# Kernel optimization log

Measured on AMD Instinct MI355X. Metric: run time of the kernel, lower is better.

## Reference

```python
import jax, jax.numpy as jnp
import numpy as np

T, B, F, H, P = 256, 512, 256, 512, 12  # seq len, batch, feature_dim, hidden_dim, p_interval


def setup_inputs() -> dict:
    key = jax.random.key(0)
    ks = jax.random.split(key, 9)
    s = 1.0 / np.sqrt(F + H)  # torch Linear default init scale
    def lin(k):
        kw, kb = jax.random.split(k)
        W = jax.random.uniform(kw, (F + H, H), jnp.float32, -s, s)
        b = jax.random.uniform(kb, (H,), jnp.float32, -s, s)
        return W, b
    Wf, bf = lin(ks[0])
    Wi, bi = lin(ks[1])
    Wo, bo = lin(ks[2])
    Wg, bg = lin(ks[3])
    x = jax.random.normal(ks[4], (T, B, F), jnp.float32)
    return {"x": x, "Wf": Wf, "bf": bf, "Wi": Wi, "bi": bi,
            "Wo": Wo, "bo": bo, "Wg": Wg, "bg": bg}


def _slstm(x, Wf, bf, Wi, bi, Wo, bo, Wg, bg):
    Tn, Bn, _ = x.shape
    h0 = jnp.zeros((P, Bn, H), x.dtype)
    # NOTE: original torch code reassigns c to a 2D [B,H] tensor after step 0,
    # so c[t % P] indexes a batch ROW (shape [H]) that broadcasts. At t=0 the
    # slice is all-zeros either way, so carrying a 2D c is exactly faithful.
    c0 = jnp.zeros((Bn, H), x.dtype)

    def step(carry, inp):
        h, c = carry
        x_t, t = inp
        idx = t % P
        xc = jnp.concatenate([x_t, h[idx]], axis=1)  # [B, F+H]
        f = jax.nn.softmax(xc @ Wf + bf, axis=1)
        i = jax.nn.softmax(xc @ Wi + bi, axis=1)
        o = jax.nn.softmax(xc @ Wo + bo, axis=1)
        g = jnp.tanh(xc @ Wg + bg)
        c_new = jnp.tanh(f * c[idx] + i * g)  # c[idx]: row [H], broadcasts over B
        h = h.at[idx].set(o * c_new)
        return (h, c_new), None

    (h, _), _ = jax.lax.scan(step, (h0, c0), (x, jnp.arange(Tn)))
    return h[(Tn - 1) % P]


def reference(x, Wf, bf, Wi, bi, Wo, bo, Wg, bg):
    return _slstm(x, Wf, bf, Wi, bi, Wo, bo, Wg, bg)
```

## Files before the change

kernel.cpp:

```cpp
#include <hip/hip_runtime.h>

typedef unsigned short u16;
typedef unsigned int   u32;

typedef __attribute__((ext_vector_type(8))) short bf16x8;
typedef __attribute__((ext_vector_type(16))) float f32x16;

__device__ __forceinline__ u16 f2bf(float v) {
    u32 u = __float_as_uint(v);
    u32 r = (u + 0x7fffu + ((u >> 16) & 1u)) >> 16;
    return (u16)r;
}
__device__ __forceinline__ float bf2f(u16 h) { return __uint_as_float(((u32)h) << 16); }

__device__ __forceinline__ float ftanh(float x) {
    float e = __expf(2.0f * x);
    return 1.0f - 2.0f * __builtin_amdgcn_rcpf(e + 1.0f);
}

__device__ __forceinline__ void gl2lds16(const void* g, void* l) {
    __builtin_amdgcn_global_load_lds(
        (const __attribute__((address_space(1))) void*)g,
        (__attribute__((address_space(3))) void*)l, 16, 0, 0);
}

__global__ void init_k(u16* __restrict__ hh, u16* __restrict__ hl, float* __restrict__ cb) {
    int i = blockIdx.x * 256 + threadIdx.x;
    hh[i] = 0; hl[i] = 0;
    if (i < 2 * 512) cb[i] = 0.0f;
}

__global__ void pack_wq(const float* __restrict__ Wf, const float* __restrict__ bf_,
                        const float* __restrict__ Wi, const float* __restrict__ bi_,
                        const float* __restrict__ Wo, const float* __restrict__ bo_,
                        const float* __restrict__ Wg, const float* __restrict__ bg_,
                        u16* __restrict__ wq, float* __restrict__ bias4) {
    int idx = blockIdx.x * 256 + threadIdx.x;
    int n = idx / 768, k = idx - n * 768;
    int gate = n >> 9, col = n & 511;
    const float* W = (gate == 0) ? Wf : (gate == 1) ? Wi : (gate == 2) ? Wo : Wg;
    float v = W[k * 512 + col];
    u16 h = f2bf(v);
    u16 l = f2bf(v - bf2f(h));
    size_t base = (size_t)n * 2304;
    if (k < 256) {
        wq[base + k] = h; wq[base + 512 + k] = h; wq[base + 256 + k] = l;
    } else {
        int d = k - 256;
        wq[base + 768 + d] = h; wq[base + 1792 + d] = h; wq[base + 1280 + d] = l;
    }
    if (k == 0) {
        const float* bb = (gate == 0) ? bf_ : (gate == 1) ? bi_ : (gate == 2) ? bo_ : bg_;
        bias4[n] = bb[col];
    }
}

__global__ void split_x(const float* __restrict__ src, u16* __restrict__ oh, u16* __restrict__ ol) {
    int i = blockIdx.x * 256 + threadIdx.x;
    float4 v = ((const float4*)src)[i];
    u16 hx = f2bf(v.x), hy = f2bf(v.y), hz = f2bf(v.z), hw = f2bf(v.w);
    u16 lx = f2bf(v.x - bf2f(hx)), ly = f2bf(v.y - bf2f(hy));
    u16 lz = f2bf(v.z - bf2f(hz)), lw = f2bf(v.w - bf2f(hw));
    uint2 hv; hv.x = (u32)hx | ((u32)hy << 16); hv.y = (u32)hz | ((u32)hw << 16);
    uint2 lv; lv.x = (u32)lx | ((u32)ly << 16); lv.y = (u32)lz | ((u32)lw << 16);
    ((uint2*)oh)[i] = hv;
    ((uint2*)ol)[i] = lv;
}

#define KT 36
__global__ __launch_bounds__(512, 2) void gemm_q(
    const u16* __restrict__ xh, const u16* __restrict__ xl,
    const u16* __restrict__ hh, const u16* __restrict__ hl,
    const u16* __restrict__ wq, const float* __restrict__ bias4,
    float* __restrict__ lg, int Mvalid, int gx) {
    __shared__ __align__(16) u16 smem[69632];

    const int tid = threadIdx.x;
    const int wid = tid >> 6, lane = tid & 63;
    const int l32 = lane & 31, khalf = lane >> 5;
    const int wm = wid >> 2, wn = wid & 3;

    int bm, bn;
    if (gx == 32) { int xcd = blockIdx.x & 7, r = blockIdx.x >> 3; bm = xcd * 4 + (r & 3); bn = r >> 2; }
    else          { bm = blockIdx.x % gx; bn = blockIdx.x / gx; }

    const int lr8 = lane >> 3;
    const int ksw = ((lane & 7) ^ (lr8 & 7)) * 8;

    int arowc[3]; size_t brow[4];
#pragma unroll
    for (int c = 0; c < 3; ++c) {
        int row = bm * 192 + (wid * 3 + c) * 8 + lr8;
        if (row >= Mvalid) row = Mvalid - 1;
        arowc[c] = row;
    }
#pragma unroll
    for (int c = 0; c < 4; ++c)
        brow[c] = (size_t)(bn * 256 + (wid * 4 + c) * 8 + lr8) * 2304;

#define STAGE_A(kt, dstoff) do {                                              \
        int kt_ = (kt); const u16* base_; int str_, ko_;                      \
        if (kt_ < 12) { base_ = (kt_ >= 8) ? xl : xh; str_ = 256; ko_ = (kt_ & 3) * 64; } \
        else { int sub_ = kt_ - 12; base_ = (sub_ >= 16) ? hl : hh; str_ = 512; ko_ = (sub_ & 7) * 64; } \
        _Pragma("unroll")                                                     \
        for (int c_ = 0; c_ < 3; ++c_)                                        \
            gl2lds16(base_ + (size_t)arowc[c_] * str_ + ko_ + ksw,            \
                     smem + (dstoff) + (wid * 3 + c_) * 512 + lane * 8);      \
    } while (0)

#define STAGE_B(kt, dstoff) do {                                              \
        _Pragma("unroll")                                                     \
        for (int c_ = 0; c_ < 4; ++c_)                                        \
            gl2lds16(wq + brow[c_] + (kt) * 64 + ksw,                         \
                     smem + (dstoff) + (wid * 4 + c_) * 512 + lane * 8);      \
    } while (0)

    u32 offA[3][4], offB[2][4];
#pragma unroll
    for (int i = 0; i < 3; ++i) {
        int row = wm * 96 + i * 32 + l32;
        u32 rsw = (u32)(row & 7) << 3;
#pragma unroll
        for (int ks = 0; ks < 4; ++ks)
            offA[i][ks] = (u32)row * 64 + (((u32)(ks * 16 + khalf * 8)) ^ rsw);
    }
#pragma unroll
    for (int j = 0; j < 2; ++j) {
        int row = wn * 64 + j * 32 + l32;
        u32 rsw = (u32)(row & 7) << 3;
#pragma unroll
        for (int ks = 0; ks < 4; ++ks)
            offB[j][ks] = (u32)row * 64 + (((u32)(ks * 16 + khalf * 8)) ^ rsw);
    }

    f32x16 acc[3][2];
#pragma unroll
    for (int i = 0; i < 3; ++i)
#pragma unroll
        for (int j = 0; j < 2; ++j)
#pragma unroll
            for (int r = 0; r < 16; ++r) acc[i][j][r] = 0.f;

    STAGE_A(0, 0);
    STAGE_B(0, 36864);
    STAGE_A(1, 12288);

    int aoff = 0;
    for (int kt = 0; kt < KT; ++kt) {
        const int boff = 36864 + ((kt & 1) << 14);
        if (kt + 1 < KT) {
            STAGE_B(kt + 1, 36864 + (((kt + 1) & 1) << 14));
            asm volatile("s_waitcnt vmcnt(7)" ::: "memory");
        } else {
            asm volatile("s_waitcnt vmcnt(0)" ::: "memory");
        }
        __builtin_amdgcn_s_barrier();
        __builtin_amdgcn_sched_barrier(0);

        const u16* At = smem + aoff;
        const u16* Bt = smem + boff;

        bf16x8 a0[3][2], b0[2][2];
#pragma unroll
        for (int i = 0; i < 3; ++i)
#pragma unroll
            for (int ks = 0; ks < 2; ++ks) a0[i][ks] = *(const bf16x8*)(At + offA[i][ks]);
#pragma unroll
        for (int j = 0; j < 2; ++j)
#pragma unroll
            for (int ks = 0; ks < 2; ++ks) b0[j][ks] = *(const bf16x8*)(Bt + offB[j][ks]);
        __builtin_amdgcn_s_setprio(1);
#pragma unroll
        for (int ks = 0; ks < 2; ++ks)
#pragma unroll
            for (int i = 0; i < 3; ++i)
#pragma unroll
                for (int j = 0; j < 2; ++j)
                    acc[i][j] = __builtin_amdgcn_mfma_f32_32x32x16_bf16(a0[i][ks], b0[j][ks], acc[i][j], 0, 0, 0);
        __builtin_amdgcn_s_setprio(0);

        if (kt + 2 < KT) {
            int adst = aoff + 24576; if (adst >= 36864) adst -= 36864;
            STAGE_A(kt + 2, adst);
        }

        bf16x8 a1[3][2], b1[2][2];
#pragma unroll
        for (int i = 0; i < 3; ++i)
#pragma unroll
            for (int ks = 0; ks < 2; ++ks) a1[i][ks] = *(const bf16x8*)(At + offA[i][ks + 2]);
#pragma unroll
        for (int j = 0; j < 2; ++j)
#pragma unroll
            for (int ks = 0; ks < 2; ++ks) b1[j][ks] = *(const bf16x8*)(Bt + offB[j][ks + 2]);
        __builtin_amdgcn_s_setprio(1);
#pragma unroll
        for (int ks = 0; ks < 2; ++ks)
#pragma unroll
            for (int i = 0; i < 3; ++i)
#pragma unroll
                for (int j = 0; j < 2; ++j)
                    acc[i][j] = __builtin_amdgcn_mfma_f32_32x32x16_bf16(a1[i][ks], b1[j][ks], acc[i][j], 0, 0, 0);
        __builtin_amdgcn_s_setprio(0);

        __builtin_amdgcn_s_barrier();
        __builtin_amdgcn_sched_barrier(0);
        aoff += 12288; if (aoff == 36864) aoff = 0;
    }
#undef STAGE_A
#undef STAGE_B

#pragma unroll
    for (int j = 0; j < 2; ++j) {
        int n = bn * 256 + wn * 64 + j * 32 + l32;
        float bv = bias4[n];
#pragma unroll
        for (int i = 0; i < 3; ++i) {
            int rbase = bm * 192 + wm * 96 + i * 32 + 4 * khalf;
#pragma unroll
            for (int r = 0; r < 16; ++r) {
                int row = rbase + (r & 3) + 8 * (r >> 2);
                if (row < Mvalid)
                    lg[(size_t)row * 2048 + n] = acc[i][j][r] + bv;
            }
        }
    }
}

__device__ __forceinline__ void chain_step(const float* __restrict__ lg, int j, int lane, float r[8]) {
    int rowb = (j + 1) % 12;
    const float* base = lg + (size_t)(j * 512 + rowb) * 2048 + lane * 8;
    float f[8], iv[8], g[8];
#pragma unroll
    for (int u = 0; u < 8; ++u) { f[u] = base[u]; iv[u] = base[512 + u]; g[u] = base[1536 + u]; }
    float mf = -1e30f, mi = -1e30f;
#pragma unroll
    for (int u = 0; u < 8; ++u) { mf = fmaxf(mf, f[u]); mi = fmaxf(mi, iv[u]); }
#pragma unroll
    for (int o = 32; o; o >>= 1) { mf = fmaxf(mf, __shfl_xor(mf, o)); mi = fmaxf(mi, __shfl_xor(mi, o)); }
    float sf = 0.f, si = 0.f;
#pragma unroll
    for (int u = 0; u < 8; ++u) {
        f[u] = __expf(f[u] - mf); sf += f[u];
        iv[u] = __expf(iv[u] - mi); si += iv[u];
    }
#pragma unroll
    for (int o = 32; o; o >>= 1) { sf += __shfl_xor(sf, o); si += __shfl_xor(si, o); }
    float rf = __builtin_amdgcn_rcpf(sf), ri = __builtin_amdgcn_rcpf(si);
#pragma unroll
    for (int u = 0; u < 8; ++u) {
        float gg = ftanh(g[u]);
        r[u] = ftanh(f[u] * rf * r[u] + iv[u] * ri * gg);
    }
}

__global__ __launch_bounds__(256) void gates_k(
    const float* __restrict__ lg, float* __restrict__ cb,
    u16* __restrict__ hh, u16* __restrict__ hl,
    float* __restrict__ out, int t0, int S, int rd, int wr) {
    __shared__ float rsh[512];
    const int widx = threadIdx.x >> 6, lane = threadIdx.x & 63;
    const int s = (S - 1) - (blockIdx.x >> 7);
    const int b = (blockIdx.x & 127) * 4 + widx;
    const int t = t0 + s;

    if (widx == 0) {
        float r[8];
#pragma unroll
        for (int u = 0; u < 8; ++u) r[u] = cb[rd * 512 + lane * 8 + u];
        for (int j = 0; j < s; ++j) chain_step(lg, j, lane, r);
#pragma unroll
        for (int u = 0; u < 8; ++u) rsh[lane * 8 + u] = r[u];
        if ((int)blockIdx.x == 127 && t0 + S < 256) {
            chain_step(lg, S - 1, lane, r);
#pragma unroll
            for (int u = 0; u < 8; ++u) cb[wr * 512 + lane * 8 + u] = r[u];
        }
    }
    __syncthreads();

    const float* row = lg + (size_t)(s * 512 + b) * 2048 + lane * 8;
    float f[8], iv[8], ov[8], g[8];
#pragma unroll
    for (int u = 0; u < 8; ++u) {
        f[u] = row[u]; iv[u] = row[512 + u]; ov[u] = row[1024 + u]; g[u] = row[1536 + u];
    }
    float mf = -1e30f, mi = -1e30f, mo = -1e30f;
#pragma unroll
    for (int u = 0; u < 8; ++u) { mf = fmaxf(mf, f[u]); mi = fmaxf(mi, iv[u]); mo = fmaxf(mo, ov[u]); }
#pragma unroll
    for (int o = 32; o; o >>= 1) {
        mf = fmaxf(mf, __shfl_xor(mf, o));
        mi = fmaxf(mi, __shfl_xor(mi, o));
        mo = fmaxf(mo, __shfl_xor(mo, o));
    }
    float sf = 0.f, si = 0.f, so = 0.f;
#pragma unroll
    for (int u = 0; u < 8; ++u) {
        f[u] = __expf(f[u] - mf); sf += f[u];
        iv[u] = __expf(iv[u] - mi); si += iv[u];
        ov[u] = __expf(ov[u] - mo); so += ov[u];
    }
#pragma unroll
    for (int o = 32; o; o >>= 1) {
        sf += __shfl_xor(sf, o); si += __shfl_xor(si, o); so += __shfl_xor(so, o);
    }
    float rf = __builtin_amdgcn_rcpf(sf), ri = __builtin_amdgcn_rcpf(si), ro = __builtin_amdgcn_rcpf(so);
    float hout[8];
#pragma unroll
    for (int u = 0; u < 8; ++u) {
        float rr = rsh[lane * 8 + u];
        float gg = ftanh(g[u]);
        float cv = ftanh(f[u] * rf * rr + iv[u] * ri * gg);
        hout[u] = ov[u] * ro * cv;
    }
    u32 hhp[4], hlp[4];
#pragma unroll
    for (int u = 0; u < 4; ++u) {
        u16 h0 = f2bf(hout[2 * u]), h1 = f2bf(hout[2 * u + 1]);
        u16 l0 = f2bf(hout[2 * u] - bf2f(h0)), l1 = f2bf(hout[2 * u + 1] - bf2f(h1));
        hhp[u] = (u32)h0 | ((u32)h1 << 16);
        hlp[u] = (u32)l0 | ((u32)l1 << 16);
    }
    size_t hb = ((size_t)(s * 512 + b)) * 512 + lane * 8;
    *(uint4*)&hh[hb] = make_uint4(hhp[0], hhp[1], hhp[2], hhp[3]);
    *(uint4*)&hl[hb] = make_uint4(hlp[0], hlp[1], hlp[2], hlp[3]);
    if (t == 255) {
        float* op = out + (size_t)b * 512 + lane * 8;
#pragma unroll
        for (int u = 0; u < 8; ++u) op[u] = hout[u];
    }
}

extern "C" void kernel_launch(void* const* d_in, const int* in_sizes, int n_in,
                              void* d_out, int out_size, void* d_ws, size_t ws_size,
                              hipStream_t stream) {
    const float* x   = (const float*)d_in[0];
    const float* Wf  = (const float*)d_in[1];
    const float* bf_ = (const float*)d_in[2];
    const float* Wi  = (const float*)d_in[3];
    const float* bi_ = (const float*)d_in[4];
    const float* Wo  = (const float*)d_in[5];
    const float* bo_ = (const float*)d_in[6];
    const float* Wg  = (const float*)d_in[7];
    const float* bg_ = (const float*)d_in[8];
    float* out = (float*)d_out;

    char* p = (char*)d_ws;
    u16* xh  = (u16*)p; p += 134217728;
    u16* xl  = (u16*)p; p += 134217728;
    u16* wq  = (u16*)p; p += 9437184;
    u16* hh  = (u16*)p; p += 6291456;
    u16* hl  = (u16*)p; p += 6291456;
    float* bias4 = (float*)p; p += 8192;
    float* cb    = (float*)p; p += 4096;
    float* lg    = (float*)p; p += 50331648;

    init_k<<<12288, 256, 0, stream>>>(hh, hl, cb);
    pack_wq<<<6144, 256, 0, stream>>>(Wf, bf_, Wi, bi_, Wo, bo_, Wg, bg_, wq, bias4);
    split_x<<<32768, 256, 0, stream>>>(x, xh, xl);

    for (int blk = 0; blk < 22; ++blk) {
        int t0 = blk * 12;
        int S = (256 - t0 >= 12) ? 12 : (256 - t0);
        int M = S * 512;
        int gx = (M + 191) / 192;
        gemm_q<<<gx * 8, 512, 0, stream>>>(
            xh + (size_t)t0 * 512 * 256, xl + (size_t)t0 * 512 * 256,
            hh, hl, wq, bias4, lg, M, gx);
        gates_k<<<S * 128, 256, 0, stream>>>(lg, cb, hh, hl, out, t0, S, blk & 1, (blk + 1) & 1);
    }
}
```

Baseline: 2.053 ms.

## Restructure GEMM main loop into four interleaved phases with split global-to-LDS staging

Splits each k-tile iteration into four sub-phases. Each phase issues its LDS fragment loads plus a slice of the next B or A tile's global-to-LDS copies, then hits a barrier and runs its MFMAs. The goal is to spread memory traffic evenly across compute instead of issuing whole-tile stages at two points. Buffer offsets are now computed from kt modulo 3 and 2, and the loop is unrolled 6 so those offsets become constants. The cost is many more workgroup barriers per k-tile, which could add synchronization stalls.

```diff
diff --git a/kernel.cpp b/kernel.cpp
--- a/kernel.cpp
+++ b/kernel.cpp
@@ -98,19 +98,19 @@
     for (int c = 0; c < 4; ++c)
         brow[c] = (size_t)(bn * 256 + (wid * 4 + c) * 8 + lr8) * 2304;
 
-#define STAGE_A(kt, dstoff) do {                                              \
+#define STAGE_A(kt, dstoff, c0, nc) do {                                      \
         int kt_ = (kt); const u16* base_; int str_, ko_;                      \
         if (kt_ < 12) { base_ = (kt_ >= 8) ? xl : xh; str_ = 256; ko_ = (kt_ & 3) * 64; } \
         else { int sub_ = kt_ - 12; base_ = (sub_ >= 16) ? hl : hh; str_ = 512; ko_ = (sub_ & 7) * 64; } \
         _Pragma("unroll")                                                     \
-        for (int c_ = 0; c_ < 3; ++c_)                                        \
+        for (int c_ = (c0); c_ < (c0) + (nc); ++c_)                           \
             gl2lds16(base_ + (size_t)arowc[c_] * str_ + ko_ + ksw,            \
                      smem + (dstoff) + (wid * 3 + c_) * 512 + lane * 8);      \
     } while (0)
 
-#define STAGE_B(kt, dstoff) do {                                              \
+#define STAGE_B(kt, dstoff, c0, nc) do {                                      \
         _Pragma("unroll")                                                     \
-        for (int c_ = 0; c_ < 4; ++c_)                                        \
+        for (int c_ = (c0); c_ < (c0) + (nc); ++c_)                           \
             gl2lds16(wq + brow[c_] + (kt) * 64 + ksw,                         \
                      smem + (dstoff) + (wid * 4 + c_) * 512 + lane * 8);      \
     } while (0)
@@ -141,71 +141,53 @@
 #pragma unroll
             for (int r = 0; r < 16; ++r) acc[i][j][r] = 0.f;
 
-    STAGE_A(0, 0);
-    STAGE_B(0, 36864);
-    STAGE_A(1, 12288);
-
-    int aoff = 0;
+    STAGE_A(0, 0, 0, 3);
+    STAGE_B(0, 36864, 0, 4);
+    STAGE_A(1, 12288, 0, 3);
+    asm volatile("s_waitcnt vmcnt(3)" ::: "memory");
+    __builtin_amdgcn_s_barrier();
+    __builtin_amdgcn_sched_barrier(0);
+
+#pragma unroll 6
     for (int kt = 0; kt < KT; ++kt) {
-        const int boff = 36864 + ((kt & 1) << 14);
-        if (kt + 1 < KT) {
-            STAGE_B(kt + 1, 36864 + (((kt + 1) & 1) << 14));
-            asm volatile("s_waitcnt vmcnt(7)" ::: "memory");
-        } else {
-            asm volatile("s_waitcnt vmcnt(0)" ::: "memory");
+        const u16* At = smem + (kt % 3) * 12288;
+        const u16* Bt = smem + 36864 + (kt & 1) * 16384;
+        const int bdst = 36864 + (((kt + 1) & 1) << 14);
+        const int adst = ((kt + 2) % 3) * 12288;
+
+#pragma unroll
+        for (int p = 0; p < 4; ++p) {
+            bf16x8 a[3], b[2];
+#pragma unroll
+            for (int i = 0; i < 3; ++i) a[i] = *(const bf16x8*)(At + offA[i][p]);
+#pragma unroll
+            for (int j = 0; j < 2; ++j) b[j] = *(const bf16x8*)(Bt + offB[j][p]);
+            if (p == 0 && kt + 1 < KT) STAGE_B(kt + 1, bdst, 0, 2);
+            if (p == 1 && kt + 1 < KT) STAGE_B(kt + 1, bdst, 2, 2);
+            if (p == 2 && kt + 2 < KT) STAGE_A(kt + 2, adst, 0, 2);
+            if (p == 3 && kt + 2 < KT) STAGE_A(kt + 2, adst, 2, 1);
+
+            __builtin_amdgcn_s_barrier();
+            __builtin_amdgcn_sched_barrier(0);
+
+            __builtin_amdgcn_s_setprio(1);
+#pragma unroll
+            for (int i = 0; i < 3; ++i)
+#pragma unroll
+                for (int j = 0; j < 2; ++j)
+                    acc[i][j] = __builtin_amdgcn_mfma_f32_32x32x16_bf16(a[i], b[j], acc[i][j], 0, 0, 0);
+            __builtin_amdgcn_s_setprio(0);
+
+            if (p < 3) {
+                __builtin_amdgcn_s_barrier();
+                __builtin_amdgcn_sched_barrier(0);
+            }
         }
+
+        if (kt < KT - 2) asm volatile("s_waitcnt vmcnt(3)" ::: "memory");
+        else             asm volatile("s_waitcnt vmcnt(0)" ::: "memory");
         __builtin_amdgcn_s_barrier();
         __builtin_amdgcn_sched_barrier(0);
-
-        const u16* At = smem + aoff;
-        const u16* Bt = smem + boff;
-
-        bf16x8 a0[3][2], b0[2][2];
-#pragma unroll
-        for (int i = 0; i < 3; ++i)
-#pragma unroll
-            for (int ks = 0; ks < 2; ++ks) a0[i][ks] = *(const bf16x8*)(At + offA[i][ks]);
-#pragma unroll
-        for (int j = 0; j < 2; ++j)
-#pragma unroll
-            for (int ks = 0; ks < 2; ++ks) b0[j][ks] = *(const bf16x8*)(Bt + offB[j][ks]);
-        __builtin_amdgcn_s_setprio(1);
-#pragma unroll
-        for (int ks = 0; ks < 2; ++ks)
-#pragma unroll
-            for (int i = 0; i < 3; ++i)
-#pragma unroll
-                for (int j = 0; j < 2; ++j)
-                    acc[i][j] = __builtin_amdgcn_mfma_f32_32x32x16_bf16(a0[i][ks], b0[j][ks], acc[i][j], 0, 0, 0);
-        __builtin_amdgcn_s_setprio(0);
-
-        if (kt + 2 < KT) {
-            int adst = aoff + 24576; if (adst >= 36864) adst -= 36864;
-            STAGE_A(kt + 2, adst);
-        }
-
-        bf16x8 a1[3][2], b1[2][2];
-#pragma unroll
-        for (int i = 0; i < 3; ++i)
-#pragma unroll
-            for (int ks = 0; ks < 2; ++ks) a1[i][ks] = *(const bf16x8*)(At + offA[i][ks + 2]);
-#pragma unroll
-        for (int j = 0; j < 2; ++j)
-#pragma unroll
-            for (int ks = 0; ks < 2; ++ks) b1[j][ks] = *(const bf16x8*)(Bt + offB[j][ks + 2]);
-        __builtin_amdgcn_s_setprio(1);
-#pragma unroll
-        for (int ks = 0; ks < 2; ++ks)
-#pragma unroll
-            for (int i = 0; i < 3; ++i)
-#pragma unroll
-                for (int j = 0; j < 2; ++j)
-                    acc[i][j] = __builtin_amdgcn_mfma_f32_32x32x16_bf16(a1[i][ks], b1[j][ks], acc[i][j], 0, 0, 0);
-        __builtin_amdgcn_s_setprio(0);
-
-        __builtin_amdgcn_s_barrier();
-        __builtin_amdgcn_sched_barrier(0);
-        aoff += 12288; if (aoff == 36864) aoff = 0;
     }
 #undef STAGE_A
 #undef STAGE_B
```

Result: faster. 1.988 ms (-3.1%).
